# Optimization experiments

Measured on AMD Instinct MI355X. Metric: run time of the kernel, lower is better.

Reference implementation:

```python
import jax, jax.numpy as jnp
import numpy as np

N_QUBITS = 10
N_LAYERS = 3


def _apply_1q(state, gate, q, batched):
    # state: (B,) + (2,)*n ; gate: (2,2) or (B,2,2)
    s = jnp.moveaxis(state, q + 1, -1)
    shp = s.shape
    s = s.reshape(shp[0], -1, 2)
    eq = 'bij,brj->bri' if batched else 'ij,brj->bri'
    s = jnp.einsum(eq, gate, s).reshape(shp)
    return jnp.moveaxis(s, -1, q + 1)


def _apply_cnot(state, c, t):
    s = jnp.moveaxis(state, (c + 1, t + 1), (-2, -1))
    s = s.at[..., 1, :].set(s[..., 1, ::-1])  # flip target where control==1
    return jnp.moveaxis(s, (-2, -1), (c + 1, t + 1))


def _rot_gate(phi, theta, omega):
    # PennyLane Rot(phi,theta,omega) = RZ(omega) @ RY(theta) @ RZ(phi)
    ch = jnp.cos(theta * 0.5).astype(jnp.complex64)
    sh = jnp.sin(theta * 0.5).astype(jnp.complex64)
    m00 = jnp.exp(-1j * (phi + omega) * 0.5) * ch
    m01 = -jnp.exp(1j * (phi - omega) * 0.5) * sh
    m10 = jnp.exp(-1j * (phi - omega) * 0.5) * sh
    m11 = jnp.exp(1j * (phi + omega) * 0.5) * ch
    return jnp.stack([jnp.stack([m00, m01]), jnp.stack([m10, m11])])


def _circuit(x, weights):
    B = x.shape[0]
    n = N_QUBITS
    state = jnp.zeros((B,) + (2,) * n, jnp.complex64)
    state = state.at[(slice(None),) + (0,) * n].set(1.0)  # |0...0>
    c = jnp.cos(x * 0.5)  # (B, n)
    s = jnp.sin(x * 0.5)
    for l in range(N_LAYERS):
        # AngleEmbedding: RY(x_q) on each wire (batched gates)
        for q in range(n):
            g = jnp.stack([jnp.stack([c[:, q], -s[:, q]], -1),
                           jnp.stack([s[:, q], c[:, q]], -1)], -2).astype(jnp.complex64)
            state = _apply_1q(state, g, q, True)
        # StronglyEntanglingLayers, single sub-layer: Rot on each wire
        for q in range(n):
            g = _rot_gate(weights[l, q, 0], weights[l, q, 1], weights[l, q, 2])
            state = _apply_1q(state, g, q, False)
        # ring of CNOTs with range r=1
        for q in range(n):
            state = _apply_cnot(state, q, (q + 1) % n)
    probs = jnp.abs(state) ** 2  # (B,) + (2,)*n, real
    outs = []
    for q in range(n):
        axes = tuple(a for a in range(1, n + 1) if a != q + 1)
        m = probs.sum(axis=axes)  # (B, 2)
        outs.append(m[:, 0] - m[:, 1])  # <Z_q>
    return jnp.stack(outs, axis=1).astype(jnp.float32)


def setup_inputs() -> dict:
    key = jax.random.key(0)
    k1, k2 = jax.random.split(key)
    x = jax.random.normal(k1, (4096, N_QUBITS), dtype=jnp.float32)
    weights = jax.random.uniform(k2, (N_LAYERS, N_QUBITS, 3), dtype=jnp.float32,
                                 minval=-np.pi, maxval=np.pi)
    return {"x": x, "weights": weights}


def reference(x, weights):
    return _circuit(x, weights)
```

## Files before the change

kernel.cpp:

```cpp
#include <hip/hip_runtime.h>

#define NQ 10
#define NL 3

typedef float v2f __attribute__((ext_vector_type(2)));

__device__ __forceinline__ int   f2i(float v) { union { float f; int i; } u; u.f = v; return u.i; }
__device__ __forceinline__ float i2f(int v)   { union { int i; float f; } u; u.i = v; return u.f; }

__device__ __forceinline__ v2f cmul(v2f a, v2f b) {
    return (v2f){ fmaf(a.x, b.x, -a.y * b.y), fmaf(a.x, b.y, a.y * b.x) };
}

template<int SP> __device__ __forceinline__ v2f pk_mul_sel(v2f a, v2f K) {
    v2f d;
    if constexpr (SP == 0)
        asm("v_pk_mul_f32 %0, %1, %2 op_sel:[0,0] op_sel_hi:[1,0]" : "=v"(d) : "v"(a), "v"(K));
    else
        asm("v_pk_mul_f32 %0, %1, %2 op_sel:[0,1] op_sel_hi:[1,1]" : "=v"(d) : "v"(a), "v"(K));
    return d;
}
template<int SP> __device__ __forceinline__ v2f pk_fma_sel(v2f a, v2f K, v2f c) {
    v2f d;
    if constexpr (SP == 0)
        asm("v_pk_fma_f32 %0, %1, %2, %3 op_sel:[0,0,0] op_sel_hi:[1,0,1]"
            : "=v"(d) : "v"(a), "v"(K), "v"(c));
    else
        asm("v_pk_fma_f32 %0, %1, %2, %3 op_sel:[0,1,0] op_sel_hi:[1,1,1]"
            : "=v"(d) : "v"(a), "v"(K), "v"(c));
    return d;
}
template<int SP> __device__ __forceinline__ v2f pk_fma_i_sel(v2f a, v2f K, v2f c) {
    v2f d;
    if constexpr (SP == 0)
        asm("v_pk_fma_f32 %0, %1, %2, %3 op_sel:[1,0,0] op_sel_hi:[0,0,1] neg_lo:[1,0,0]"
            : "=v"(d) : "v"(a), "v"(K), "v"(c));
    else
        asm("v_pk_fma_f32 %0, %1, %2, %3 op_sel:[1,1,0] op_sel_hi:[0,1,1] neg_lo:[1,0,0]"
            : "=v"(d) : "v"(a), "v"(K), "v"(c));
    return d;
}

template<int LM>
__device__ __forceinline__ v2f xlane(v2f v, int baddr) {
    int x = f2i(v.x), y = f2i(v.y);
    if constexpr (LM == 1) {
        x = __builtin_amdgcn_mov_dpp(x, 177, 0xF, 0xF, false);
        y = __builtin_amdgcn_mov_dpp(y, 177, 0xF, 0xF, false);
    } else if constexpr (LM == 2) {
        x = __builtin_amdgcn_mov_dpp(x, 78, 0xF, 0xF, false);
        y = __builtin_amdgcn_mov_dpp(y, 78, 0xF, 0xF, false);
    } else if constexpr (LM == 3) {
        x = __builtin_amdgcn_mov_dpp(x, 27, 0xF, 0xF, false);
        y = __builtin_amdgcn_mov_dpp(y, 27, 0xF, 0xF, false);
    } else if constexpr (LM < 32) {
        constexpr int off = (LM << 10) | 0x1F;
        x = __builtin_amdgcn_ds_swizzle(x, off);
        y = __builtin_amdgcn_ds_swizzle(y, off);
    } else {
        x = __builtin_amdgcn_ds_bpermute(baddr, x);
        y = __builtin_amdgcn_ds_bpermute(baddr, y);
    }
    return (v2f){ i2f(x), i2f(y) };
}

template<int MASK, int RMASK>
__device__ __forceinline__ void apply_gate(v2f (&a)[16], float4 r0, float4 r1,
                                           float cq, float sq, int lane)
{
    constexpr int LM = (MASK >> 4) & 63;
    constexpr int JM = MASK & 15;
    constexpr int RH = (RMASK >> 4) & 63;
    constexpr int RL = RMASK & 15;

    const float g00r = fmaf(r0.x, cq,  r0.z * sq), g00i = fmaf(r0.y, cq,  r0.w * sq);
    const float g01r = fmaf(r0.z, cq, -r0.x * sq), g01i = fmaf(r0.w, cq, -r0.y * sq);
    const float g10r = fmaf(r1.x, cq,  r1.z * sq), g10i = fmaf(r1.y, cq,  r1.w * sq);
    const float g11r = fmaf(r1.z, cq, -r1.x * sq), g11i = fmaf(r1.w, cq, -r1.y * sq);

    const int lp = (RH != 0) ? (__popc(lane & RH) & 1) : 0;
    const v2f KAr = lp ? (v2f){g11r, g00r} : (v2f){g00r, g11r};
    const v2f KAi = lp ? (v2f){g11i, g00i} : (v2f){g00i, g11i};
    const v2f KBr = lp ? (v2f){g10r, g01r} : (v2f){g01r, g10r};
    const v2f KBi = lp ? (v2f){g10i, g01i} : (v2f){g01i, g10i};

    const int baddr = ((lane ^ LM) << 2);

    if constexpr (JM == 0) {
#define QNN_X(J)                                                              \
        { constexpr int SP_ = __builtin_popcount((J) & RL) & 1;               \
          v2f o_ = xlane<LM>(a[J], baddr);                                    \
          v2f t_ = pk_mul_sel<SP_>(a[J], KAr);                                \
          t_ = pk_fma_i_sel<SP_>(a[J], KAi, t_);                              \
          t_ = pk_fma_sel<SP_>(o_, KBr, t_);                                  \
          t_ = pk_fma_i_sel<SP_>(o_, KBi, t_);                                \
          a[J] = t_; }
        QNN_X(0) QNN_X(1) QNN_X(2) QNN_X(3) QNN_X(4) QNN_X(5) QNN_X(6) QNN_X(7)
        QNN_X(8) QNN_X(9) QNN_X(10) QNN_X(11) QNN_X(12) QNN_X(13) QNN_X(14) QNN_X(15)
#undef QNN_X
    } else {
        constexpr int HB = 1 << (31 - __builtin_clz((unsigned)JM));
#define QNN_P(J)                                                              \
        if constexpr (((J) & HB) == 0) {                                      \
            constexpr int K_  = (J) ^ JM;                                     \
            constexpr int SPJ = __builtin_popcount((J) & RL) & 1;             \
            constexpr int SPK = __builtin_popcount(K_  & RL) & 1;             \
            v2f aj_ = a[J], ak_ = a[K_];                                      \
            v2f oj_, ok_;                                                     \
            if constexpr (LM != 0) { oj_ = xlane<LM>(ak_, baddr);             \
                                     ok_ = xlane<LM>(aj_, baddr); }           \
            else                   { oj_ = ak_; ok_ = aj_; }                  \
            { v2f t_ = pk_mul_sel<SPJ>(aj_, KAr);                             \
              t_ = pk_fma_i_sel<SPJ>(aj_, KAi, t_);                           \
              t_ = pk_fma_sel<SPJ>(oj_, KBr, t_);                             \
              t_ = pk_fma_i_sel<SPJ>(oj_, KBi, t_);  a[J]  = t_; }            \
            { v2f t_ = pk_mul_sel<SPK>(ak_, KAr);                             \
              t_ = pk_fma_i_sel<SPK>(ak_, KAi, t_);                           \
              t_ = pk_fma_sel<SPK>(ok_, KBr, t_);                             \
              t_ = pk_fma_i_sel<SPK>(ok_, KBi, t_);  a[K_] = t_; }            \
        }
        QNN_P(0) QNN_P(1) QNN_P(2) QNN_P(3) QNN_P(4) QNN_P(5) QNN_P(6) QNN_P(7)
        QNN_P(8) QNN_P(9) QNN_P(10) QNN_P(11) QNN_P(12) QNN_P(13) QNN_P(14) QNN_P(15)
#undef QNN_P
    }
}

__global__ __launch_bounds__(256, 4)
void qnn_kernel(const float* __restrict__ x, const float* __restrict__ w,
                float* __restrict__ out)
{
    __shared__ float4 rotL[NL * NQ][2];

    const int t    = threadIdx.x;
    const int lane = t & 63;
    const int b    = blockIdx.x * 4 + (t >> 6);

    if (t < NL * NQ) {
        const float* wp = w + t * 3;
        float phi = wp[0], th = wp[1], om = wp[2];
        float ct = cosf(th * 0.5f), st = sinf(th * 0.5f);
        float ap = (phi + om) * 0.5f, am = (phi - om) * 0.5f;
        float cap = cosf(ap), sap = sinf(ap);
        float cam = cosf(am), sam = sinf(am);
        rotL[t][0] = make_float4(cap * ct, -sap * ct, -cam * st, -sam * st);
        rotL[t][1] = make_float4(cam * st, -sam * st,  cap * ct,  sap * ct);
    }
    __syncthreads();

    const float* xb = x + (size_t)__builtin_amdgcn_readfirstlane(b * NQ);
    float c_[NQ], s_[NQ];
    #pragma unroll
    for (int q = 0; q < NQ; ++q) {
        float xv = xb[q] * 0.5f;
        c_[q] = __cosf(xv);
        s_[q] = __sinf(xv);
    }

    v2f c0[4], c1[4];
    v2f Ln = {1.f, 0.f};
    #pragma unroll
    for (int q = 0; q < NQ; ++q) {
        float4 r0 = rotL[q][0], r1 = rotL[q][1];
        float cq = c_[q], sq = s_[q];
        v2f g0 = { fmaf(r0.x, cq, r0.z * sq), fmaf(r0.y, cq, r0.w * sq) };
        v2f g1 = { fmaf(r1.x, cq, r1.z * sq), fmaf(r1.y, cq, r1.w * sq) };
        if (q < 4) { c0[q] = g0; c1[q] = g1; }
        else {
            v2f gg = ((lane >> (q - 4)) & 1) ? g1 : g0;
            Ln = (q == 4) ? gg : cmul(Ln, gg);
        }
    }
    v2f S01[4], SH[4];
    #pragma unroll
    for (int j = 0; j < 4; ++j)
        S01[j] = cmul((j & 1) ? c1[0] : c0[0], (j & 2) ? c1[1] : c0[1]);
    #pragma unroll
    for (int h = 0; h < 4; ++h)
        SH[h] = cmul(cmul((h & 1) ? c1[2] : c0[2], (h & 2) ? c1[3] : c0[3]), Ln);
    v2f a[16];
    #pragma unroll
    for (int j = 0; j < 16; ++j)
        a[j] = cmul(S01[j & 3], SH[j >> 2]);

#define GATE(IDX, Q, MASK, RMASK) \
    apply_gate<MASK, RMASK>(a, rotL[IDX][0], rotL[IDX][1], c_[Q], s_[Q], lane);
    GATE(10, 0, 0x003, 0x3FE)  GATE(11, 1, 0x006, 0x003)
    GATE(12, 2, 0x00C, 0x007)  GATE(13, 3, 0x018, 0x00F)
    GATE(14, 4, 0x030, 0x01F)  GATE(15, 5, 0x060, 0x03F)
    GATE(16, 6, 0x0C0, 0x07F)  GATE(17, 7, 0x180, 0x0FF)
    GATE(18, 8, 0x300, 0x1FF)  GATE(19, 9, 0x203, 0x3FF)
    GATE(20, 0, 0x005, 0x2AB)  GATE(21, 1, 0x00A, 0x3FD)
    GATE(22, 2, 0x014, 0x3FA)  GATE(23, 3, 0x028, 0x3F5)
    GATE(24, 4, 0x050, 0x3EA)  GATE(25, 5, 0x0A0, 0x3D5)
    GATE(26, 6, 0x140, 0x3AA)  GATE(27, 7, 0x280, 0x355)
    GATE(28, 8, 0x103, 0x2AA)  GATE(29, 9, 0x206, 0x155)
#undef GATE

    float P[16];
    #pragma unroll
    for (int j = 0; j < 16; ++j)
        P[j] = fmaf(a[j].x, a[j].x, a[j].y * a[j].y);
    #pragma unroll
    for (int bit = 0; bit < 4; ++bit) {
        #pragma unroll
        for (int j = 0; j < 16; ++j)
            if (!(j & (1 << bit))) {
                int k = j | (1 << bit);
                float u = P[j], v = P[k];
                P[j] = u + v;
                P[k] = u - v;
            }
    }

    const int bp32 = ((lane ^ 32) << 2);
    float vout = 0.f;
#define MEAS(Q, RM)                                                           \
    { constexpr int RH_ = ((RM) >> 4) & 63;                                   \
      constexpr int RL_ = (RM) & 15;                                          \
      float v = P[RL_];                                                       \
      if (__popc(lane & RH_) & 1) v = -v;                                     \
      v += i2f(__builtin_amdgcn_mov_dpp(f2i(v), 177, 0xF, 0xF, false));       \
      v += i2f(__builtin_amdgcn_mov_dpp(f2i(v), 78, 0xF, 0xF, false));        \
      v += i2f(__builtin_amdgcn_ds_swizzle(f2i(v), (4 << 10) | 0x1F));        \
      v += i2f(__builtin_amdgcn_ds_swizzle(f2i(v), (8 << 10) | 0x1F));        \
      v += i2f(__builtin_amdgcn_ds_swizzle(f2i(v), (16 << 10) | 0x1F));       \
      v += i2f(__builtin_amdgcn_ds_bpermute(bp32, f2i(v)));                   \
      if (lane == (Q)) vout = v; }
    MEAS(0, 0x0CD) MEAS(1, 0x156) MEAS(2, 0x2AC) MEAS(3, 0x159)
    MEAS(4, 0x2B3) MEAS(5, 0x166) MEAS(6, 0x2CC) MEAS(7, 0x199)
    MEAS(8, 0x333) MEAS(9, 0x266)
#undef MEAS

    if (lane < NQ) out[b * NQ + lane] = vout;
}

extern "C" void kernel_launch(void* const* d_in, const int* in_sizes, int n_in,
                              void* d_out, int out_size, void* d_ws, size_t ws_size,
                              hipStream_t stream) {
    const float* x = (const float*)d_in[0];
    const float* w = (const float*)d_in[1];
    float* out = (float*)d_out;
    const int B = in_sizes[0] / NQ;
    qnn_kernel<<<B / 4, 256, 0, stream>>>(x, w, out);
}
```

Before: 79.17 us.

## Split each circuit state across two waves with LDS exchange for top qubit

Each sample's 1024-amplitude state now spans a 128-thread block (two wavefronts), with 8 amplitudes per lane instead of 16, and one qubit is mapped to the wave index. Gates that touch that qubit exchange amplitudes through shared memory with block barriers, and the final Z expectations are summed across the two waves via LDS. This halves per-thread register work and increases the number of parallel waves, at the cost of LDS staging, extra syncthreads on three gates, and duplicated per-sample setup (trig, rotation precompute) in twice as many threads.

```diff
diff --git a/kernel.cpp b/kernel.cpp
--- a/kernel.cpp
+++ b/kernel.cpp
@@ -1,7 +1,6 @@
 #include <hip/hip_runtime.h>
 
 #define NQ 10
-#define NL 3
 
 typedef float v2f __attribute__((ext_vector_type(2)));
 
@@ -43,6 +42,7 @@
 
 template<int LM>
 __device__ __forceinline__ v2f xlane(v2f v, int baddr) {
+    if constexpr (LM == 0) return v;
     int x = f2i(v.x), y = f2i(v.y);
     if constexpr (LM == 1) {
         x = __builtin_amdgcn_mov_dpp(x, 177, 0xF, 0xF, false);
@@ -64,78 +64,84 @@
     return (v2f){ i2f(x), i2f(y) };
 }
 
-template<int MASK, int RMASK>
-__device__ __forceinline__ void apply_gate(v2f (&a)[16], float4 r0, float4 r1,
-                                           float cq, float sq, int lane)
-{
-    constexpr int LM = (MASK >> 4) & 63;
-    constexpr int JM = MASK & 15;
-    constexpr int RH = (RMASK >> 4) & 63;
-    constexpr int RL = RMASK & 15;
-
+struct Kset { v2f Ar, Ai, Br, Bi; };
+
+__device__ __forceinline__ Kset build_K(float4 r0, float4 r1, float cq, float sq, int lp)
+{
     const float g00r = fmaf(r0.x, cq,  r0.z * sq), g00i = fmaf(r0.y, cq,  r0.w * sq);
     const float g01r = fmaf(r0.z, cq, -r0.x * sq), g01i = fmaf(r0.w, cq, -r0.y * sq);
     const float g10r = fmaf(r1.x, cq,  r1.z * sq), g10i = fmaf(r1.y, cq,  r1.w * sq);
     const float g11r = fmaf(r1.z, cq, -r1.x * sq), g11i = fmaf(r1.w, cq, -r1.y * sq);
-
-    const int lp = (RH != 0) ? (__popc(lane & RH) & 1) : 0;
-    const v2f KAr = lp ? (v2f){g11r, g00r} : (v2f){g00r, g11r};
-    const v2f KAi = lp ? (v2f){g11i, g00i} : (v2f){g00i, g11i};
-    const v2f KBr = lp ? (v2f){g10r, g01r} : (v2f){g01r, g10r};
-    const v2f KBi = lp ? (v2f){g10i, g01i} : (v2f){g01i, g10i};
-
-    const int baddr = ((lane ^ LM) << 2);
-
-    if constexpr (JM == 0) {
-#define QNN_X(J)                                                              \
-        { constexpr int SP_ = __builtin_popcount((J) & RL) & 1;               \
-          v2f o_ = xlane<LM>(a[J], baddr);                                    \
-          v2f t_ = pk_mul_sel<SP_>(a[J], KAr);                                \
-          t_ = pk_fma_i_sel<SP_>(a[J], KAi, t_);                              \
-          t_ = pk_fma_sel<SP_>(o_, KBr, t_);                                  \
-          t_ = pk_fma_i_sel<SP_>(o_, KBi, t_);                                \
-          a[J] = t_; }
-        QNN_X(0) QNN_X(1) QNN_X(2) QNN_X(3) QNN_X(4) QNN_X(5) QNN_X(6) QNN_X(7)
-        QNN_X(8) QNN_X(9) QNN_X(10) QNN_X(11) QNN_X(12) QNN_X(13) QNN_X(14) QNN_X(15)
-#undef QNN_X
-    } else {
-        constexpr int HB = 1 << (31 - __builtin_clz((unsigned)JM));
-#define QNN_P(J)                                                              \
-        if constexpr (((J) & HB) == 0) {                                      \
-            constexpr int K_  = (J) ^ JM;                                     \
-            constexpr int SPJ = __builtin_popcount((J) & RL) & 1;             \
-            constexpr int SPK = __builtin_popcount(K_  & RL) & 1;             \
-            v2f aj_ = a[J], ak_ = a[K_];                                      \
-            v2f oj_, ok_;                                                     \
-            if constexpr (LM != 0) { oj_ = xlane<LM>(ak_, baddr);             \
-                                     ok_ = xlane<LM>(aj_, baddr); }           \
-            else                   { oj_ = ak_; ok_ = aj_; }                  \
-            { v2f t_ = pk_mul_sel<SPJ>(aj_, KAr);                             \
-              t_ = pk_fma_i_sel<SPJ>(aj_, KAi, t_);                           \
-              t_ = pk_fma_sel<SPJ>(oj_, KBr, t_);                             \
-              t_ = pk_fma_i_sel<SPJ>(oj_, KBi, t_);  a[J]  = t_; }            \
-            { v2f t_ = pk_mul_sel<SPK>(ak_, KAr);                             \
-              t_ = pk_fma_i_sel<SPK>(ak_, KAi, t_);                           \
-              t_ = pk_fma_sel<SPK>(ok_, KBr, t_);                             \
-              t_ = pk_fma_i_sel<SPK>(ok_, KBi, t_);  a[K_] = t_; }            \
-        }
-        QNN_P(0) QNN_P(1) QNN_P(2) QNN_P(3) QNN_P(4) QNN_P(5) QNN_P(6) QNN_P(7)
-        QNN_P(8) QNN_P(9) QNN_P(10) QNN_P(11) QNN_P(12) QNN_P(13) QNN_P(14) QNN_P(15)
-#undef QNN_P
-    }
-}
-
-__global__ __launch_bounds__(256, 4)
+    Kset K;
+    K.Ar = lp ? (v2f){g11r, g00r} : (v2f){g00r, g11r};
+    K.Ai = lp ? (v2f){g11i, g00i} : (v2f){g00i, g11i};
+    K.Br = lp ? (v2f){g10r, g01r} : (v2f){g01r, g10r};
+    K.Bi = lp ? (v2f){g10i, g01i} : (v2f){g01i, g10i};
+    return K;
+}
+
+#define QNN_FMA8                                                              \
+    QNN_F(0) QNN_F(1) QNN_F(2) QNN_F(3) QNN_F(4) QNN_F(5) QNN_F(6) QNN_F(7)
+#define QNN_F(J) { constexpr int SP_ = __builtin_popcount((J) & RJ) & 1;      \
+    v2f t_ = pk_mul_sel<SP_>(a[J], K.Ar);                                     \
+    t_ = pk_fma_i_sel<SP_>(a[J], K.Ai, t_);                                   \
+    t_ = pk_fma_sel<SP_>(o[J], K.Br, t_);                                     \
+    t_ = pk_fma_i_sel<SP_>(o[J], K.Bi, t_);                                   \
+    a[J] = t_; }
+
+template<int M, int RJ, int RL, int RW>
+__device__ __forceinline__ void gate_reg(v2f (&a)[8], float4 r0, float4 r1,
+                                         float cq, float sq, int lane, int wv)
+{
+    constexpr int JM = M & 7;
+    constexpr int LM = (M >> 3) & 63;
+    int lp = 0;
+    if constexpr (RL != 0) lp = __popc(lane & RL) & 1;
+    if constexpr (RW != 0) lp ^= wv;
+    const Kset K = build_K(r0, r1, cq, sq, lp);
+    const int baddr = (lane ^ LM) << 2;
+    v2f o[8];
+    #pragma unroll
+    for (int j = 0; j < 8; ++j) o[j] = xlane<LM>(a[j ^ JM], baddr);
+    QNN_FMA8
+}
+
+template<int M, int RJ, int RL, int RW>
+__device__ __forceinline__ void gate_wm(v2f (&a)[8], v2f* stage, float4 r0, float4 r1,
+                                        float cq, float sq, int tid, int wv)
+{
+    constexpr int JM = M & 7;
+    constexpr int LW = (M >> 3) & 127;
+    const int lane = tid & 63;
+    int lp = 0;
+    if constexpr (RL != 0) lp = __popc(lane & RL) & 1;
+    if constexpr (RW != 0) lp ^= wv;
+    const Kset K = build_K(r0, r1, cq, sq, lp);
+    #pragma unroll
+    for (int j = 0; j < 8; ++j) stage[j * 128 + tid] = a[j];
+    __syncthreads();
+    const int pt = tid ^ LW;
+    v2f o[8];
+    #pragma unroll
+    for (int j = 0; j < 8; ++j) o[j] = stage[(j ^ JM) * 128 + pt];
+    __syncthreads();
+    QNN_FMA8
+}
+
+__global__ __launch_bounds__(128, 8)
 void qnn_kernel(const float* __restrict__ x, const float* __restrict__ w,
                 float* __restrict__ out)
 {
-    __shared__ float4 rotL[NL * NQ][2];
+    __shared__ float4 rotL[3 * NQ][2];
+    __shared__ v2f    stage[1024];
+    __shared__ float  zred[2][NQ];
 
     const int t    = threadIdx.x;
     const int lane = t & 63;
-    const int b    = blockIdx.x * 4 + (t >> 6);
-
-    if (t < NL * NQ) {
+    const int wv   = t >> 6;
+    const int b    = blockIdx.x;
+
+    if (t < 3 * NQ) {
         const float* wp = w + t * 3;
         float phi = wp[0], th = wp[1], om = wp[2];
         float ct = cosf(th * 0.5f), st = sinf(th * 0.5f);
@@ -147,63 +153,73 @@
     }
     __syncthreads();
 
-    const float* xb = x + (size_t)__builtin_amdgcn_readfirstlane(b * NQ);
+    const float* xb = x + (size_t)(b * NQ);
     float c_[NQ], s_[NQ];
     #pragma unroll
     for (int q = 0; q < NQ; ++q) {
         float xv = xb[q] * 0.5f;
-        c_[q] = __cosf(xv);
-        s_[q] = __sinf(xv);
-    }
-
-    v2f c0[4], c1[4];
-    v2f Ln = {1.f, 0.f};
+        c_[q] = i2f(__builtin_amdgcn_readfirstlane(f2i(__cosf(xv))));
+        s_[q] = i2f(__builtin_amdgcn_readfirstlane(f2i(__sinf(xv))));
+    }
+
+    v2f tq[3][2], Ln, Wf;
     #pragma unroll
     for (int q = 0; q < NQ; ++q) {
-        float4 r0 = rotL[q][0], r1 = rotL[q][1];
-        float cq = c_[q], sq = s_[q];
+        const float4 r0 = rotL[q][0], r1 = rotL[q][1];
+        const float cq = c_[q], sq = s_[q];
         v2f g0 = { fmaf(r0.x, cq, r0.z * sq), fmaf(r0.y, cq, r0.w * sq) };
         v2f g1 = { fmaf(r1.x, cq, r1.z * sq), fmaf(r1.y, cq, r1.w * sq) };
-        if (q < 4) { c0[q] = g0; c1[q] = g1; }
-        else {
-            v2f gg = ((lane >> (q - 4)) & 1) ? g1 : g0;
-            Ln = (q == 4) ? gg : cmul(Ln, gg);
-        }
-    }
-    v2f S01[4], SH[4];
+        if (q < 3)      { tq[q][0] = g0; tq[q][1] = g1; }
+        else if (q < 9) { v2f gg = ((lane >> (q - 3)) & 1) ? g1 : g0;
+                          Ln = (q == 3) ? gg : cmul(Ln, gg); }
+        else            { Wf = wv ? g1 : g0; }
+    }
+    const v2f LWp = cmul(Ln, Wf);
+    v2f S01[4];
     #pragma unroll
     for (int j = 0; j < 4; ++j)
-        S01[j] = cmul((j & 1) ? c1[0] : c0[0], (j & 2) ? c1[1] : c0[1]);
-    #pragma unroll
-    for (int h = 0; h < 4; ++h)
-        SH[h] = cmul(cmul((h & 1) ? c1[2] : c0[2], (h & 2) ? c1[3] : c0[3]), Ln);
-    v2f a[16];
-    #pragma unroll
-    for (int j = 0; j < 16; ++j)
+        S01[j] = cmul(tq[0][j & 1], tq[1][(j >> 1) & 1]);
+    const v2f SH[2] = { cmul(tq[2][0], LWp), cmul(tq[2][1], LWp) };
+    v2f a[8];
+    #pragma unroll
+    for (int j = 0; j < 8; ++j)
         a[j] = cmul(S01[j & 3], SH[j >> 2]);
 
-#define GATE(IDX, Q, MASK, RMASK) \
-    apply_gate<MASK, RMASK>(a, rotL[IDX][0], rotL[IDX][1], c_[Q], s_[Q], lane);
-    GATE(10, 0, 0x003, 0x3FE)  GATE(11, 1, 0x006, 0x003)
-    GATE(12, 2, 0x00C, 0x007)  GATE(13, 3, 0x018, 0x00F)
-    GATE(14, 4, 0x030, 0x01F)  GATE(15, 5, 0x060, 0x03F)
-    GATE(16, 6, 0x0C0, 0x07F)  GATE(17, 7, 0x180, 0x0FF)
-    GATE(18, 8, 0x300, 0x1FF)  GATE(19, 9, 0x203, 0x3FF)
-    GATE(20, 0, 0x005, 0x2AB)  GATE(21, 1, 0x00A, 0x3FD)
-    GATE(22, 2, 0x014, 0x3FA)  GATE(23, 3, 0x028, 0x3F5)
-    GATE(24, 4, 0x050, 0x3EA)  GATE(25, 5, 0x0A0, 0x3D5)
-    GATE(26, 6, 0x140, 0x3AA)  GATE(27, 7, 0x280, 0x355)
-    GATE(28, 8, 0x103, 0x2AA)  GATE(29, 9, 0x206, 0x155)
-#undef GATE
-
-    float P[16];
-    #pragma unroll
-    for (int j = 0; j < 16; ++j)
+#define GR(IDX, Q, M, RJ, RL, RW) \
+    gate_reg<M, RJ, RL, RW>(a, rotL[IDX][0], rotL[IDX][1], c_[Q], s_[Q], lane, wv);
+#define GW(IDX, Q, M, RJ, RL, RW) \
+    gate_wm<M, RJ, RL, RW>(a, stage, rotL[IDX][0], rotL[IDX][1], c_[Q], s_[Q], t, wv);
+    GR(10, 0, 0x003, 6, 63, 1)
+    GR(11, 1, 0x006, 3,  0, 0)
+    GR(12, 2, 0x00C, 7,  0, 0)
+    GR(13, 3, 0x018, 7,  1, 0)
+    GR(14, 4, 0x030, 7,  3, 0)
+    GR(15, 5, 0x060, 7,  7, 0)
+    GR(16, 6, 0x0C0, 7, 15, 0)
+    GR(17, 7, 0x180, 7, 31, 0)
+    GW(18, 8, 0x300, 7, 63, 0)
+    GW(19, 9, 0x203, 7, 63, 1)
+    GR(20, 0, 0x005, 3, 21, 1)
+    GR(21, 1, 0x00A, 5, 63, 1)
+    GR(22, 2, 0x014, 2, 63, 1)
+    GR(23, 3, 0x028, 5, 62, 1)
+    GR(24, 4, 0x050, 2, 61, 1)
+    GR(25, 5, 0x0A0, 5, 58, 1)
+    GR(26, 6, 0x140, 2, 53, 1)
+    GW(27, 7, 0x280, 5, 42, 1)
+    GR(28, 8, 0x103, 2, 21, 1)
+    GW(29, 9, 0x206, 5, 42, 0)
+#undef GR
+#undef GW
+
+    float P[8];
+    #pragma unroll
+    for (int j = 0; j < 8; ++j)
         P[j] = fmaf(a[j].x, a[j].x, a[j].y * a[j].y);
     #pragma unroll
-    for (int bit = 0; bit < 4; ++bit) {
+    for (int bit = 0; bit < 3; ++bit) {
         #pragma unroll
-        for (int j = 0; j < 16; ++j)
+        for (int j = 0; j < 8; ++j)
             if (!(j & (1 << bit))) {
                 int k = j | (1 << bit);
                 float u = P[j], v = P[k];
@@ -214,11 +230,11 @@
 
     const int bp32 = ((lane ^ 32) << 2);
     float vout = 0.f;
-#define MEAS(Q, RM)                                                           \
-    { constexpr int RH_ = ((RM) >> 4) & 63;                                   \
-      constexpr int RL_ = (RM) & 15;                                          \
-      float v = P[RL_];                                                       \
-      if (__popc(lane & RH_) & 1) v = -v;                                     \
+#define MEAS(Q, RJ_, RL_, RW_)                                                \
+    { float v = P[RJ_];                                                       \
+      int ng = __popc(lane & (RL_)) & 1;                                      \
+      if (RW_) ng ^= wv;                                                      \
+      if (ng) v = -v;                                                         \
       v += i2f(__builtin_amdgcn_mov_dpp(f2i(v), 177, 0xF, 0xF, false));       \
       v += i2f(__builtin_amdgcn_mov_dpp(f2i(v), 78, 0xF, 0xF, false));        \
       v += i2f(__builtin_amdgcn_ds_swizzle(f2i(v), (4 << 10) | 0x1F));        \
@@ -226,12 +242,14 @@
       v += i2f(__builtin_amdgcn_ds_swizzle(f2i(v), (16 << 10) | 0x1F));       \
       v += i2f(__builtin_amdgcn_ds_bpermute(bp32, f2i(v)));                   \
       if (lane == (Q)) vout = v; }
-    MEAS(0, 0x0CD) MEAS(1, 0x156) MEAS(2, 0x2AC) MEAS(3, 0x159)
-    MEAS(4, 0x2B3) MEAS(5, 0x166) MEAS(6, 0x2CC) MEAS(7, 0x199)
-    MEAS(8, 0x333) MEAS(9, 0x266)
+    MEAS(0, 5, 25, 0) MEAS(1, 6, 42, 0) MEAS(2, 4, 21, 1) MEAS(3, 1, 43, 0)
+    MEAS(4, 3, 22, 1) MEAS(5, 6, 44, 0) MEAS(6, 4, 25, 1) MEAS(7, 1, 51, 0)
+    MEAS(8, 3, 38, 1) MEAS(9, 6, 12, 1)
 #undef MEAS
 
-    if (lane < NQ) out[b * NQ + lane] = vout;
+    if (lane < NQ) zred[wv][lane] = vout;
+    __syncthreads();
+    if (t < NQ) out[b * NQ + t] = zred[0][t] + zred[1][t];
 }
 
 extern "C" void kernel_launch(void* const* d_in, const int* in_sizes, int n_in,
@@ -241,5 +259,5 @@
     const float* w = (const float*)d_in[1];
     float* out = (float*)d_out;
     const int B = in_sizes[0] / NQ;
-    qnn_kernel<<<B / 4, 256, 0, stream>>>(x, w, out);
-}
+    qnn_kernel<<<B, 128, 0, stream>>>(x, w, out);
+}
```

Measured after the change: 82.69 us. +4.5%, slower.
